# Kernel tuning notes

Measured on AMD Instinct MI355X. Metric: run time of the kernel, lower is better.

Reference implementation:

```python
import jax, jax.numpy as jnp
import numpy as np

B, DIM, L, H, W = 4, 128, 256, 8, 8
N = L * H * W
D_INNER, D_STATE, D_CONV, DT_RANK = 128, 8, 4, 8


def _ln(x, w, b, eps=1e-5):
    m = x.mean(-1, keepdims=True)
    v = ((x - m) ** 2).mean(-1, keepdims=True)
    return (x - m) * jax.lax.rsqrt(v + eps) * w + b


def _mamba_fusion(x, z_in, p, i):
    # x, z_in: (B, N, DIM). x drives the SSM; z_in provides the cross-modal gate.
    u = x @ p['Wx'][i]                                    # (B, N, D_INNER)
    z = z_in @ p['Wz'][i]                                 # (B, N, D_INNER)
    # causal depthwise conv1d along tokens, kernel D_CONV (torch pad=k-1 then truncate)
    up = jnp.pad(u, ((0, 0), (D_CONV - 1, 0), (0, 0)))
    w = p['conv_w'][i]                                    # (D_INNER, D_CONV)
    uc = sum(up[:, k:k + u.shape[1], :] * w[:, k] for k in range(D_CONV)) + p['conv_b'][i]
    uc = jax.nn.silu(uc)
    x_dbl = uc @ p['Wxproj'][i]                           # (B, N, DT_RANK + 2*D_STATE)
    dt_r, Bm, Cm = jnp.split(x_dbl, [DT_RANK, DT_RANK + D_STATE], axis=-1)
    dt = jax.nn.softplus(dt_r @ p['Wdt'][i] + p['bdt'][i])  # (B, N, D_INNER)
    A = -jnp.exp(p['A_log'][i])                           # (D_INNER, D_STATE)
    dA = jnp.exp(dt[..., None] * A)                       # (B, N, D_INNER, D_STATE)
    dBu = dt[..., None] * Bm[:, :, None, :] * uc[..., None]

    def step(h, inp):
        dA_t, dBu_t, C_t = inp
        h = dA_t * h + dBu_t                              # (B, D_INNER, D_STATE)
        return h, jnp.einsum('bds,bs->bd', h, C_t)

    h0 = jnp.zeros((u.shape[0], D_INNER, D_STATE), u.dtype)
    _, ys = jax.lax.scan(step, h0, (dA.swapaxes(0, 1), dBu.swapaxes(0, 1), Cm.swapaxes(0, 1)))
    y = ys.swapaxes(0, 1) + p['Dp'][i] * uc
    y = y * jax.nn.silu(z)
    return y @ p['Wout_m'][i] + p['bout_m'][i]


def _cross_block(in0, in1, p, i):
    skip = in0
    a = _ln(in0, p['ln0_w'][i], p['ln0_b'][i])
    b = _ln(in1, p['ln1_w'][i], p['ln1_b'][i])
    return skip + _mamba_fusion(a, b, p, i)


def setup_inputs() -> dict:
    key = jax.random.key(0)
    ks = jax.random.split(key, 16)
    s_in = 1.0 / np.sqrt(DIM)
    s_di = 1.0 / np.sqrt(D_INNER)
    inp = {
        'front': jax.random.normal(ks[0], (B, DIM, L, H, W), jnp.float32),
        'back': jax.random.normal(ks[1], (B, DIM, L, H, W), jnp.float32),
        'ln0_w': jnp.ones((2, DIM), jnp.float32),
        'ln0_b': jnp.zeros((2, DIM), jnp.float32),
        'ln1_w': jnp.ones((2, DIM), jnp.float32),
        'ln1_b': jnp.zeros((2, DIM), jnp.float32),
        'Wx': jax.random.normal(ks[2], (2, DIM, D_INNER), jnp.float32) * s_in,
        'Wz': jax.random.normal(ks[3], (2, DIM, D_INNER), jnp.float32) * s_in,
        'conv_w': jax.random.normal(ks[4], (2, D_INNER, D_CONV), jnp.float32) * 0.5,
        'conv_b': jnp.zeros((2, D_INNER), jnp.float32),
        'Wxproj': jax.random.normal(ks[5], (2, D_INNER, DT_RANK + 2 * D_STATE), jnp.float32) * s_di,
        'Wdt': jax.random.normal(ks[6], (2, DT_RANK, D_INNER), jnp.float32) * (1.0 / np.sqrt(DT_RANK)),
        'bdt': jnp.full((2, D_INNER), -4.6, jnp.float32),  # softplus^-1(~0.01)
        'A_log': jnp.broadcast_to(jnp.log(jnp.arange(1, D_STATE + 1, dtype=jnp.float32)), (2, D_INNER, D_STATE)).copy(),
        'Dp': jnp.ones((2, D_INNER), jnp.float32),
        'Wout_m': jax.random.normal(ks[7], (2, D_INNER, DIM), jnp.float32) * s_di,
        'bout_m': jnp.zeros((2, DIM), jnp.float32),
        'Wout': jax.random.normal(ks[8], (DIM, DIM), jnp.float32) * s_in,
        'bout': jnp.zeros((DIM,), jnp.float32),
    }
    return inp


def reference(front, back, ln0_w, ln0_b, ln1_w, ln1_b, Wx, Wz, conv_w, conv_b,
              Wxproj, Wdt, bdt, A_log, Dp, Wout_m, bout_m, Wout, bout):
    p = dict(ln0_w=ln0_w, ln0_b=ln0_b, ln1_w=ln1_w, ln1_b=ln1_b, Wx=Wx, Wz=Wz,
             conv_w=conv_w, conv_b=conv_b, Wxproj=Wxproj, Wdt=Wdt, bdt=bdt,
             A_log=A_log, Dp=Dp, Wout_m=Wout_m, bout_m=bout_m)
    ff = front.reshape(B, DIM, N).swapaxes(1, 2)          # (B, N, DIM)
    bf = back.reshape(B, DIM, N).swapaxes(1, 2)
    f_fus = _cross_block(ff, bf, p, 0)
    b_fus = _cross_block(bf, ff, p, 1)
    fusion = ((f_fus + b_fus) * 0.5) @ Wout + bout
    return fusion.swapaxes(1, 2).reshape(B, DIM, L, H, W)
```

## Files before the change

kernel.cpp:

```cpp
#include <hip/hip_runtime.h>

#define DEV static __device__ __forceinline__

typedef short s16x8 __attribute__((ext_vector_type(8)));
typedef float f32x4 __attribute__((ext_vector_type(4)));
typedef unsigned short u16;

DEV float b2f(u16 u){ return __uint_as_float(((unsigned int)u) << 16); }
DEV u16 f2b(float f){
  unsigned int x = __float_as_uint(f);
  x += 0x7fffu + ((x >> 16) & 1u);
  return (u16)(x >> 16);
}
DEV float silu_f(float x){ return x * __builtin_amdgcn_rcpf(1.f + __expf(-x)); }
DEV float softplus_f(float x){ return (x > 15.f) ? x : __logf(1.f + __expf(x)); }
DEV bool detf32(const void* lnw){ return *(const unsigned int*)lnw == 0x3F800000u; }
DEV float ldin(const void* p, long long i, bool f){
  return f ? ((const float*)p)[i] : b2f(((const u16*)p)[i]);
}

static constexpr int BATCH = 4;
static constexpr int NSEQ  = 16384;
static constexpr int RTOT  = BATCH * NSEQ;
static constexpr int GCH   = 256;
static constexpr int DIRSZ = BATCH*GCH*128*8;

DEV int swz(int row, int col){ return (row << 7) + (col ^ ((row & 7) << 3)); }

__global__ __launch_bounds__(256) void k_setup(
                        const void* ln0w, const void* ln0b, const void* ln1w, const void* ln1b,
                        const void* Wx, const void* Wz, const void* Wxp, const void* Wdt,
                        const void* bdt, const void* Alog, const void* convw, const void* convb,
                        const void* Dpr, const void* Woutm, const void* boutm,
                        const void* Wout, const void* bout,
                        u16* Wuz, u16* WdtBC, u16* Wcat, u16* WoutT,
                        float* buz, float* bdtf, float* bcat, float* boutf,
                        float* Aexp, float* convwF, float* convbF, float* DpF)
{
  bool f = detf32(ln0w);
  int tid = blockIdx.x * 256 + threadIdx.x;
  int gs  = gridDim.x * 256;
  for (int idx = tid; idx < 2*256*128; idx += gs){
    int d = idx >> 15; int n = (idx >> 7) & 255; int k = idx & 127;
    float wv;
    if (n < 128) wv = ldin(ln0w, d*128+k, f) * ldin(Wx, (long long)(d*128+k)*128 + n, f);
    else         wv = ldin(ln1w, (1-d)*128+k, f) * ldin(Wz, (long long)((1-d)*128+k)*128 + (n-128), f);
    Wuz[idx] = f2b(wv);
  }
  for (int idx = tid; idx < 2*256; idx += gs){
    int d = idx >> 8; int n = idx & 255;
    float s = 0.f;
    if (n < 128){
      for (int k = 0; k < 128; ++k)
        s += ldin(ln0b, d*128+k, f) * ldin(Wx, (long long)(d*128+k)*128 + n, f);
    } else {
      for (int k = 0; k < 128; ++k)
        s += ldin(ln1b, (1-d)*128+k, f) * ldin(Wz, (long long)((1-d)*128+k)*128 + (n-128), f);
    }
    buz[idx] = s;
  }
  for (int idx = tid; idx < 2*128; idx += gs)
    bdtf[idx] = ldin(bdt, idx, f);
  for (int idx = tid; idx < 2*144*128; idx += gs){
    int i = idx / (144*128); int rem = idx % (144*128); int n = rem >> 7; int k = rem & 127;
    if (n < 128){
      float s = 0.f;
      for (int j = 0; j < 8; ++j)
        s += ldin(Wxp, (long long)(i*128+k)*24 + j, f) * ldin(Wdt, (long long)(i*8+j)*128 + n, f);
      WdtBC[idx] = f2b(s);
    } else {
      WdtBC[idx] = f2b(ldin(Wxp, (long long)(i*128+k)*24 + (n - 120), f));
    }
  }
  for (int idx = tid; idx < 128*256; idx += gs){
    int n = idx >> 8; int k = idx & 255;
    Wcat[idx] = f2b(ldin(Woutm, (long long)k*128 + n, f));
  }
  for (int idx = tid; idx < 128*128; idx += gs){
    int n = idx >> 7, k = idx & 127;
    WoutT[idx] = f2b(ldin(Wout, (long long)k*128 + n, f));
  }
  for (int idx = tid; idx < 128; idx += gs){
    bcat[idx]  = ldin(boutm, idx, f) + ldin(boutm, 128 + idx, f);
    boutf[idx] = ldin(bout, idx, f);
  }
  for (int idx = tid; idx < 2*128*8; idx += gs)
    Aexp[idx] = -expf(ldin(Alog, idx, f));
  for (int idx = tid; idx < 2*128*4; idx += gs)
    convwF[idx] = ldin(convw, idx, f);
  for (int idx = tid; idx < 2*128; idx += gs){
    convbF[idx] = ldin(convb, idx, f);
    DpF[idx]   = ldin(Dpr, idx, f);
  }
}

__global__ __launch_bounds__(256) void k_ln(const void* front, const void* back, const void* ln0w,
                                            u16* xf, u16* xb, u16* sfbh)
{
  bool fF = detf32(ln0w);
  __shared__ u16 Af[64][130];
  __shared__ u16 Ab[64][130];
  __shared__ float Mf[64], Rf[64], Mb[64], Rb[64];
  int tid = threadIdx.x;
  long long r0 = (long long)blockIdx.x * 64;
  int b  = (int)(r0 >> 14);
  int n0 = (int)(r0 & 16383);
  if (fF){
    const float* fp = (const float*)front;
    const float* bp = (const float*)back;
    for (int it = 0; it < 8; ++it){
      int d = it*16 + (tid >> 4);
      int t = (tid & 15) * 4;
      long long gi = ((long long)(b*128 + d))*NSEQ + n0 + t;
      float4 vf = *(const float4*)&fp[gi];
      float4 vb = *(const float4*)&bp[gi];
      Af[t+0][d] = f2b(vf.x); Af[t+1][d] = f2b(vf.y);
      Af[t+2][d] = f2b(vf.z); Af[t+3][d] = f2b(vf.w);
      Ab[t+0][d] = f2b(vb.x); Ab[t+1][d] = f2b(vb.y);
      Ab[t+2][d] = f2b(vb.z); Ab[t+3][d] = f2b(vb.w);
    }
  } else {
    const u16* fp = (const u16*)front;
    const u16* bp = (const u16*)back;
    for (int it = 0; it < 4; ++it){
      int d = it*32 + (tid >> 3);
      int t = (tid & 7) * 8;
      long long gi = ((long long)(b*128 + d))*NSEQ + n0 + t;
      uint4 vf = *(const uint4*)&fp[gi];
      uint4 vb = *(const uint4*)&bp[gi];
      Af[t+0][d] = (u16)vf.x; Af[t+1][d] = (u16)(vf.x>>16);
      Af[t+2][d] = (u16)vf.y; Af[t+3][d] = (u16)(vf.y>>16);
      Af[t+4][d] = (u16)vf.z; Af[t+5][d] = (u16)(vf.z>>16);
      Af[t+6][d] = (u16)vf.w; Af[t+7][d] = (u16)(vf.w>>16);
      Ab[t+0][d] = (u16)vb.x; Ab[t+1][d] = (u16)(vb.x>>16);
      Ab[t+2][d] = (u16)vb.y; Ab[t+3][d] = (u16)(vb.y>>16);
      Ab[t+4][d] = (u16)vb.z; Ab[t+5][d] = (u16)(vb.z>>16);
      Ab[t+6][d] = (u16)vb.w; Ab[t+7][d] = (u16)(vb.w>>16);
    }
  }
  __syncthreads();
  {
    int t = tid >> 2, sub = tid & 3;
    float s = 0.f, ss = 0.f, s2 = 0.f, ss2 = 0.f;
    for (int k = 0; k < 32; ++k){
      float v = b2f(Af[t][sub*32 + k]); s  += v; ss  += v*v;
      float w = b2f(Ab[t][sub*32 + k]); s2 += w; ss2 += w*w;
    }
    for (int m = 1; m < 4; m <<= 1){
      s  += __shfl_xor(s,  m, 64); ss  += __shfl_xor(ss,  m, 64);
      s2 += __shfl_xor(s2, m, 64); ss2 += __shfl_xor(ss2, m, 64);
    }
    if (sub == 0){
      float mf = s  * (1.f/128.f); float vf = ss  * (1.f/128.f) - mf*mf;
      Mf[t] = mf; Rf[t] = rsqrtf(vf + 1e-5f);
      float mb = s2 * (1.f/128.f); float vb = ss2 * (1.f/128.f) - mb*mb;
      Mb[t] = mb; Rb[t] = rsqrtf(vb + 1e-5f);
    }
  }
  __syncthreads();
  for (int it = 0; it < 8; ++it){
    int t = it*8 + (tid >> 5);
    int c = (tid & 31) * 4;
    float mf = Mf[t], rf = Rf[t], mb = Mb[t], rb = Rb[t];
    float f0 = b2f(Af[t][c+0]), f1 = b2f(Af[t][c+1]), f2 = b2f(Af[t][c+2]), f3 = b2f(Af[t][c+3]);
    float g0 = b2f(Ab[t][c+0]), g1 = b2f(Ab[t][c+1]), g2 = b2f(Ab[t][c+2]), g3 = b2f(Ab[t][c+3]);
    ushort4 xo, zo, so;
    xo.x = f2b((f0-mf)*rf); xo.y = f2b((f1-mf)*rf); xo.z = f2b((f2-mf)*rf); xo.w = f2b((f3-mf)*rf);
    zo.x = f2b((g0-mb)*rb); zo.y = f2b((g1-mb)*rb); zo.z = f2b((g2-mb)*rb); zo.w = f2b((g3-mb)*rb);
    so.x = f2b(f0+g0); so.y = f2b(f1+g1); so.z = f2b(f2+g2); so.w = f2b(f3+g3);
    long long o = (r0 + t)*128 + c;
    *(ushort4*)&xf[o] = xo;
    *(ushort4*)&xb[o] = zo;
    *(ushort4*)&sfbh[o] = so;
  }
}

__global__ __launch_bounds__(256) void k_guz(const u16* __restrict__ xf,
                                             const u16* __restrict__ xb,
                                             const u16* __restrict__ Wuz,
                                             const float* __restrict__ buz,
                                             u16* __restrict__ u0, u16* __restrict__ u1,
                                             u16* __restrict__ z0, u16* __restrict__ z1)
{
  int dir = blockIdx.y;
  const u16* A = dir ? xb : xf;
  const u16* Wt = Wuz + dir*256*128;
  const float* bias = buz + dir*256;
  u16* outU = dir ? u1 : u0;
  u16* outZ = dir ? z0 : z1;
  __shared__ u16 Wl[256][72];
  __shared__ u16 Al[64][72];
  int tid = threadIdx.x;
  long long r0 = (long long)blockIdx.x * 64;
  int w = tid >> 6, lane = tid & 63;
  int q = lane >> 4, m = lane & 15;
  f32x4 acc[16];
  #pragma unroll
  for (int ct = 0; ct < 16; ++ct) acc[ct] = (f32x4){0.f,0.f,0.f,0.f};
  for (int kp = 0; kp < 2; ++kp){
    if (kp) __syncthreads();
    for (int ci = tid; ci < 256*8; ci += 256){
      int n = ci >> 3, c8 = ci & 7;
      *(uint4*)&Wl[n][c8*8] = *(const uint4*)&Wt[n*128 + kp*64 + c8*8];
    }
    for (int ci = tid; ci < 64*8; ci += 256){
      int rl = ci >> 3, c8 = ci & 7;
      *(uint4*)&Al[rl][c8*8] = *(const uint4*)&A[(r0 + rl)*128 + kp*64 + c8*8];
    }
    __syncthreads();
    #pragma unroll
    for (int kt = 0; kt < 2; ++kt){
      s16x8 af = *(const s16x8*)&Al[w*16 + m][kt*32 + q*8];
      #pragma unroll
      for (int ct = 0; ct < 16; ++ct){
        s16x8 bf = *(const s16x8*)&Wl[ct*16 + m][kt*32 + q*8];
        acc[ct] = __builtin_amdgcn_mfma_f32_16x16x32_bf16(af, bf, acc[ct], 0, 0, 0);
      }
    }
  }
  #pragma unroll
  for (int ct = 0; ct < 16; ++ct){
    int col = ct*16 + m;
    #pragma unroll
    for (int i = 0; i < 4; ++i){
      long long r = r0 + w*16 + q*4 + i;
      float v = acc[ct][i] + bias[col];
      if (col < 128) outU[r*128 + col] = f2b(v);
      else           outZ[r*128 + (col - 128)] = f2b(silu_f(v));
    }
  }
}

__global__ __launch_bounds__(256, 3) void k_cps(const u16* __restrict__ u0p,
                                             const u16* __restrict__ u1p,
                                             const float* __restrict__ convwF,
                                             const float* __restrict__ convbF,
                                             const u16* __restrict__ WdtBC,
                                             const float* __restrict__ bdtf,
                                             const float* __restrict__ Aexp,
                                             u16* __restrict__ uc0p, u16* __restrict__ uc1p,
                                             u16* __restrict__ yg,
                                             float* __restrict__ BCg,
                                             float* __restrict__ P, float* __restrict__ Q)
{
  __shared__ __align__(16) u16 AlF[64*128];
  __shared__ __align__(16) u16 WlF[144*128];
  int dir = blockIdx.y;
  const u16* u = dir ? u1p : u0p;
  u16* ucb = dir ? uc1p : uc0p;
  const u16* Wt = WdtBC + dir*18432;
  const float* bias = bdtf + dir*128;
  u16* dtb = yg + dir*128;
  float* BC = BCg + (long long)dir*RTOT*16;
  int tid = threadIdx.x;
  long long r0 = (long long)blockIdx.x * 64;
  int b  = (int)(r0 >> 14);
  int n0 = (int)(r0 & 16383);
  for (int ci = tid; ci < 144*16; ci += 256){
    int n = ci >> 4, c8 = ci & 15;
    *(uint4*)&WlF[(n << 7) + ((c8 ^ (n & 7)) << 3)] = *(const uint4*)&Wt[n*128 + c8*8];
  }
  {
    int c = tid & 127, h = tid >> 7;
    const float* wp = &convwF[(dir*128 + c)*4];
    float w0 = wp[0], w1 = wp[1], w2 = wp[2], w3 = wp[3];
    float cb = convbF[dir*128 + c];
    int t0 = h*32;
    const u16* up = u + (long long)b*NSEQ*128 + c;
    int nbase = n0 + t0;
    float win0 = (nbase-3 >= 0) ? b2f(up[(long long)(nbase-3)*128]) : 0.f;
    float win1 = (nbase-2 >= 0) ? b2f(up[(long long)(nbase-2)*128]) : 0.f;
    float win2 = (nbase-1 >= 0) ? b2f(up[(long long)(nbase-1)*128]) : 0.f;
    #pragma unroll
    for (int t = 0; t < 32; ++t){
      float cur = b2f(up[(long long)(nbase + t)*128]);
      float a = win0*w0 + win1*w1 + win2*w2 + cur*w3 + cb;
      u16 s = f2b(silu_f(a));
      AlF[swz(t0 + t, c)] = s;
      ucb[(r0 + t0 + t)*128 + c] = s;
      win0 = win1; win1 = win2; win2 = cur;
    }
  }
  __syncthreads();
  int w = tid >> 6, lane = tid & 63;
  int q = lane >> 4, m = lane & 15;
  f32x4 acc[9];
  #pragma unroll
  for (int ct = 0; ct < 9; ++ct) acc[ct] = (f32x4){0.f,0.f,0.f,0.f};
  #pragma unroll
  for (int kt = 0; kt < 4; ++kt){
    int sc = (kt*32 + q*8) ^ ((m & 7) << 3);
    s16x8 af = *(const s16x8*)&AlF[((w*16 + m) << 7) + sc];
    #pragma unroll
    for (int ct = 0; ct < 9; ++ct){
      s16x8 bf = *(const s16x8*)&WlF[((ct*16 + m) << 7) + sc];
      acc[ct] = __builtin_amdgcn_mfma_f32_16x16x32_bf16(af, bf, acc[ct], 0, 0, 0);
    }
  }
  __syncthreads();
  u16* Dl = WlF;
  float* BCl = (float*)&WlF[64*128];
  #pragma unroll
  for (int ct = 0; ct < 9; ++ct){
    int col = ct*16 + m;
    #pragma unroll
    for (int i = 0; i < 4; ++i){
      int rl = w*16 + q*4 + i;
      long long r = r0 + rl;
      float v = acc[ct][i];
      if (col < 128){
        u16 dv = f2b(softplus_f(v + bias[col]));
        dtb[r*256 + col] = dv;
        Dl[swz(rl, col)] = dv;
      } else {
        BC[r*16 + (col - 128)] = v;
        BCl[rl*16 + (col - 128)] = v;
      }
    }
  }
  __syncthreads();
  {
    int c = tid & 127, sh = tid >> 7;
    int g = (int)(r0 & 16383) >> 6;
    int base = sh*4;
    float Ac[4], Pr[4], H[4];
    bool fast = true;
    #pragma unroll
    for (int j = 0; j < 4; ++j){
      Ac[j] = Aexp[(dir*128 + c)*8 + base + j];
      fast = fast && (fabsf(Ac[j] + (float)(base + j + 1)) < 2e-4f);
      Pr[j] = 1.f; H[j] = 0.f;
    }
    if (fast){
      for (int t = 0; t < 64; ++t){
        int ce = swz(t, c);
        float d  = b2f(Dl[ce]);
        float uu = b2f(AlF[ce]);
        float du = d * uu;
        float E  = __expf(-d);
        float E2 = E*E, E3 = E2*E, E4 = E2*E2;
        float M  = base ? E4 : 1.f;
        float dA0 = M*E, dA1 = M*E2, dA2 = M*E3, dA3 = M*E4;
        H[0] = dA0*H[0] + du*BCl[t*16 + base+0]; Pr[0] *= dA0;
        H[1] = dA1*H[1] + du*BCl[t*16 + base+1]; Pr[1] *= dA1;
        H[2] = dA2*H[2] + du*BCl[t*16 + base+2]; Pr[2] *= dA2;
        H[3] = dA3*H[3] + du*BCl[t*16 + base+3]; Pr[3] *= dA3;
      }
    } else {
      for (int t = 0; t < 64; ++t){
        int ce = swz(t, c);
        float d  = b2f(Dl[ce]);
        float uu = b2f(AlF[ce]);
        float du = d * uu;
        #pragma unroll
        for (int j = 0; j < 4; ++j){
          float dA = __expf(d * Ac[j]);
          H[j]  = dA*H[j] + du*BCl[t*16 + base + j];
          Pr[j] *= dA;
        }
      }
    }
    long long o = (long long)dir*DIRSZ + (((long long)b*GCH + g)*128 + c)*8 + base;
    *(float4*)&P[o] = make_float4(Pr[0],Pr[1],Pr[2],Pr[3]);
    *(float4*)&Q[o] = make_float4(H[0],H[1],H[2],H[3]);
  }
}

__global__ __launch_bounds__(64) void k_scan2(const float* __restrict__ P,
                                              const float* __restrict__ Q,
                                              float* __restrict__ hinit)
{
  int idx = blockIdx.x*64 + threadIdx.x;
  int dir = idx >> 12;
  int rem = idx & 4095;
  int b  = rem >> 10;
  int cs = rem & 1023;
  long long base = (long long)dir*DIRSZ + (long long)b*GCH*1024 + cs;
  float h = 0.f;
  for (int g = 0; g < GCH; g += 8){
    long long o = base + (long long)g*1024;
    float p[8], qv[8];
    #pragma unroll
    for (int j = 0; j < 8; ++j){ p[j] = P[o + j*1024]; qv[j] = Q[o + j*1024]; }
    #pragma unroll
    for (int j = 0; j < 8; ++j){
      hinit[o + j*1024] = h;
      h = p[j]*h + qv[j];
    }
  }
}

__global__ __launch_bounds__(256) void k_scan3(const u16* __restrict__ uc0p,
                                               const u16* __restrict__ uc1p,
                                               const float* __restrict__ BCg,
                                               const float* __restrict__ hinit,
                                               const u16* __restrict__ z0p,
                                               const u16* __restrict__ z1p,
                                               const float* __restrict__ DpF,
                                               const float* __restrict__ Aexp,
                                               u16* yg)
{
  __shared__ float Bl[128][8];
  __shared__ float Cl[128][8];
  int dir = blockIdx.y;
  const u16* uc = dir ? uc1p : uc0p;
  const u16* zs = dir ? z1p : z0p;
  const float* BC = BCg + (long long)dir*RTOT*16;
  int tid = threadIdx.x;
  int gp = blockIdx.x & 127;
  int b  = blockIdx.x >> 7;
  long long tokbase = (long long)b*NSEQ + gp*128;
  for (int idx = tid; idx < 128*8; idx += 256){
    int row = idx >> 3, s = idx & 7;
    Bl[row][s] = BC[(tokbase + row)*16 + s];
    Cl[row][s] = BC[(tokbase + row)*16 + 8 + s];
  }
  __syncthreads();
  int c = tid & 127;
  int gh = tid >> 7;
  int g = gp*2 + gh;
  int doff = dir*128;
  float Ac[8], H[8];
  long long ho = (long long)dir*DIRSZ + (((long long)b*GCH + g)*128 + c)*8;
  float4 h0 = *(const float4*)&hinit[ho];
  float4 h1 = *(const float4*)&hinit[ho + 4];
  H[0]=h0.x; H[1]=h0.y; H[2]=h0.z; H[3]=h0.w;
  H[4]=h1.x; H[5]=h1.y; H[6]=h1.z; H[7]=h1.w;
  bool fast = true;
  #pragma unroll
  for (int s = 0; s < 8; ++s){
    Ac[s] = Aexp[(dir*128 + c)*8 + s];
    fast = fast && (fabsf(Ac[s] + (float)(s + 1)) < 2e-4f);
  }
  float dpc = DpF[dir*128 + c];
  long long rbase = (long long)b*NSEQ + g*64;
  if (fast){
    for (int t = 0; t < 64; ++t){
      long long r = rbase + t;
      float d  = b2f(yg[r*256 + doff + c]);
      float uu = b2f(uc[r*128 + c]);
      float du = d * uu;
      int rowl = gh*64 + t;
      float E  = __expf(-d);
      float E2 = E*E, E3 = E2*E, E4 = E2*E2;
      float dA[8] = {E, E2, E3, E4, E4*E, E4*E2, E4*E3, E4*E4};
      float y = 0.f;
      #pragma unroll
      for (int s = 0; s < 8; ++s){
        H[s] = dA[s]*H[s] + du*Bl[rowl][s];
        y += H[s]*Cl[rowl][s];
      }
      float zv = b2f(zs[r*128 + c]);
      yg[r*256 + doff + c] = f2b((y + dpc*uu) * zv);
    }
  } else {
    for (int t = 0; t < 64; ++t){
      long long r = rbase + t;
      float d  = b2f(yg[r*256 + doff + c]);
      float uu = b2f(uc[r*128 + c]);
      float du = d * uu;
      int rowl = gh*64 + t;
      float y = 0.f;
      #pragma unroll
      for (int s = 0; s < 8; ++s){
        float dA = __expf(d * Ac[s]);
        H[s] = dA*H[s] + du*Bl[rowl][s];
        y += H[s]*Cl[rowl][s];
      }
      float zv = b2f(zs[r*128 + c]);
      yg[r*256 + doff + c] = f2b((y + dpc*uu) * zv);
    }
  }
}

__global__ __launch_bounds__(256) void k_tail(const u16* __restrict__ yg,
                                              const u16* __restrict__ Wcat,
                                              const float* __restrict__ bcat,
                                              const u16* __restrict__ sfbh,
                                              const u16* __restrict__ WoutT,
                                              const float* __restrict__ boutf,
                                              void* outp, const void* dflag)
{
  __shared__ u16 Wl[128][136];
  __shared__ u16 Al[64][136];
  __shared__ u16 Sl[64][136];
  int tid = threadIdx.x;
  long long r0 = (long long)blockIdx.x * 64;
  int w = tid >> 6, lane = tid & 63;
  int q = lane >> 4, m = lane & 15;
  f32x4 acc[8];
  #pragma unroll
  for (int ct = 0; ct < 8; ++ct) acc[ct] = (f32x4){0.f,0.f,0.f,0.f};
  for (int kp = 0; kp < 2; ++kp){
    if (kp) __syncthreads();
    for (int ci = tid; ci < 128*16; ci += 256){
      int n = ci >> 4, c8 = ci & 15;
      *(uint4*)&Wl[n][c8*8] = *(const uint4*)&Wcat[n*256 + kp*128 + c8*8];
    }
    for (int ci = tid; ci < 64*16; ci += 256){
      int rl = ci >> 4, c8 = ci & 15;
      *(uint4*)&Al[rl][c8*8] = *(const uint4*)&yg[(r0 + rl)*256 + kp*128 + c8*8];
    }
    __syncthreads();
    #pragma unroll
    for (int kt = 0; kt < 4; ++kt){
      s16x8 af = *(const s16x8*)&Al[w*16 + m][kt*32 + q*8];
      #pragma unroll
      for (int ct = 0; ct < 8; ++ct){
        s16x8 bf = *(const s16x8*)&Wl[ct*16 + m][kt*32 + q*8];
        acc[ct] = __builtin_amdgcn_mfma_f32_16x16x32_bf16(af, bf, acc[ct], 0, 0, 0);
      }
    }
  }
  #pragma unroll
  for (int ct = 0; ct < 8; ++ct){
    int col = ct*16 + m;
    #pragma unroll
    for (int i = 0; i < 4; ++i){
      int rl = w*16 + q*4 + i;
      long long r = r0 + rl;
      Sl[rl][col] = f2b(acc[ct][i] + bcat[col] + b2f(sfbh[r*128 + col]));
    }
  }
  __syncthreads();
  for (int ci = tid; ci < 128*16; ci += 256){
    int n = ci >> 4, c8 = ci & 15;
    *(uint4*)&Wl[n][c8*8] = *(const uint4*)&WoutT[n*128 + c8*8];
  }
  __syncthreads();
  f32x4 acc2[8];
  #pragma unroll
  for (int ct = 0; ct < 8; ++ct) acc2[ct] = (f32x4){0.f,0.f,0.f,0.f};
  #pragma unroll
  for (int kt = 0; kt < 4; ++kt){
    s16x8 af = *(const s16x8*)&Sl[w*16 + m][kt*32 + q*8];
    #pragma unroll
    for (int ct = 0; ct < 8; ++ct){
      s16x8 bf = *(const s16x8*)&Wl[ct*16 + m][kt*32 + q*8];
      acc2[ct] = __builtin_amdgcn_mfma_f32_16x16x32_bf16(af, bf, acc2[ct], 0, 0, 0);
    }
  }
  u16* Tl = &Al[0][0];
  #pragma unroll
  for (int ct = 0; ct < 8; ++ct){
    int col = ct*16 + m;
    #pragma unroll
    for (int i = 0; i < 4; ++i){
      int rl = w*16 + q*4 + i;
      Tl[col*68 + rl] = f2b(0.5f*acc2[ct][i] + boutf[col]);
    }
  }
  __syncthreads();
  long long b = r0 >> 14; long long tok0 = r0 & 16383;
  bool fo = detf32(dflag);
  if (fo){
    float* of = (float*)outp;
    for (int idx = tid; idx < 128*16; idx += 256){
      int n = idx >> 4; int t0 = (idx & 15)*4;
      float4 v;
      v.x = b2f(Tl[n*68 + t0+0]); v.y = b2f(Tl[n*68 + t0+1]);
      v.z = b2f(Tl[n*68 + t0+2]); v.w = b2f(Tl[n*68 + t0+3]);
      *(float4*)&of[(((long long)(b*128 + n)) << 14) + tok0 + t0] = v;
    }
  } else {
    u16* ob = (u16*)outp;
    for (int idx = tid; idx < 128*16; idx += 256){
      int n = idx >> 4; int t0 = (idx & 15)*4;
      ushort4 v;
      v.x = Tl[n*68 + t0+0]; v.y = Tl[n*68 + t0+1];
      v.z = Tl[n*68 + t0+2]; v.w = Tl[n*68 + t0+3];
      *(ushort4*)&ob[(((long long)(b*128 + n)) << 14) + tok0 + t0] = v;
    }
  }
}

extern "C" void kernel_launch(void* const* d_in, const int* in_sizes, int n_in,
                              void* d_out, int out_size, void* d_ws, size_t ws_size,
                              hipStream_t stream)
{
  (void)in_sizes; (void)n_in; (void)out_size; (void)ws_size;
  const void* front = d_in[0];
  const void* back  = d_in[1];
  const void* ln0w  = d_in[2];
  const void* ln0b  = d_in[3];
  const void* ln1w  = d_in[4];
  const void* ln1b  = d_in[5];
  const void* Wx    = d_in[6];
  const void* Wz    = d_in[7];
  const void* convw = d_in[8];
  const void* convb = d_in[9];
  const void* Wxp   = d_in[10];
  const void* Wdt   = d_in[11];
  const void* bdt   = d_in[12];
  const void* Alog  = d_in[13];
  const void* Dpr   = d_in[14];
  const void* Woutm = d_in[15];
  const void* boutm = d_in[16];
  const void* Wout  = d_in[17];
  const void* bout  = d_in[18];

  char* p = (char*)d_ws;
  auto alloc = [&](size_t bytes) -> void* {
    void* q = (void*)p; p += (bytes + 255) & ~(size_t)255; return q;
  };
  u16*   xf    = (u16*)  alloc((size_t)RTOT*128*2);
  u16*   xb    = (u16*)  alloc((size_t)RTOT*128*2);
  u16*   sfbh  = (u16*)  alloc((size_t)RTOT*128*2);
  u16*   u0    = (u16*)  alloc((size_t)RTOT*128*2);
  u16*   u1    = (u16*)  alloc((size_t)RTOT*128*2);
  u16*   z0    = (u16*)  alloc((size_t)RTOT*128*2);
  u16*   z1    = (u16*)  alloc((size_t)RTOT*128*2);
  float* BC    = (float*)alloc((size_t)2*RTOT*16*4);
  float* Pb    = (float*)alloc((size_t)2*DIRSZ*4);
  float* Qb    = (float*)alloc((size_t)2*DIRSZ*4);
  float* hin   = (float*)alloc((size_t)2*DIRSZ*4);
  u16*   yg    = (u16*)  alloc((size_t)RTOT*256*2);
  u16*   Wuz   = (u16*)  alloc(2*256*128*2);
  u16*   WdtBC = (u16*)  alloc(2*144*128*2);
  u16*   Wcat  = (u16*)  alloc(128*256*2);
  u16*   WoutT = (u16*)  alloc(128*128*2);
  float* buz   = (float*)alloc(2*256*4);
  float* bdtf  = (float*)alloc(2*128*4);
  float* bcat  = (float*)alloc(128*4);
  float* boutf = (float*)alloc(128*4);
  float* Aexp  = (float*)alloc(2*128*8*4);
  float* convwF= (float*)alloc(2*128*4*4);
  float* convbF= (float*)alloc(2*128*4);
  float* DpF   = (float*)alloc(2*128*4);

  k_setup<<<128,256,0,stream>>>(ln0w,ln0b,ln1w,ln1b,Wx,Wz,Wxp,Wdt,bdt,Alog,convw,convb,Dpr,
                                Woutm,boutm,Wout,bout,
                                Wuz,WdtBC,Wcat,WoutT,buz,bdtf,bcat,boutf,Aexp,
                                convwF,convbF,DpF);
  k_ln<<<RTOT/64,256,0,stream>>>(front,back,ln0w,xf,xb,sfbh);

  dim3 g2(RTOT/64, 2);
  k_guz<<<g2,256,0,stream>>>(xf, xb, Wuz, buz, u0, u1, z0, z1);
  k_cps<<<g2,256,0,stream>>>(u0, u1, convwF, convbF, WdtBC, bdtf, Aexp,
                             xf, xb, yg, BC, Pb, Qb);
  k_scan2<<<128,64,0,stream>>>(Pb, Qb, hin);
  dim3 g3(BATCH*GCH/2, 2);
  k_scan3<<<g3,256,0,stream>>>(xf, xb, BC, hin, z0, z1, DpF, Aexp, yg);
  k_tail<<<RTOT/64,256,0,stream>>>(yg, Wcat, bcat, sfbh, WoutT, boutf, d_out, ln0w);
}
```

Before: 329.4 us.

## Fuse chunk-local scan output into conv kernel and apply carry correction in tail

```diff
diff --git a/kernel.cpp b/kernel.cpp
--- a/kernel.cpp
+++ b/kernel.cpp
@@ -1,4 +1,5 @@
 #include <hip/hip_runtime.h>
+#include <hip/hip_fp16.h>
 
 #define DEV static __device__ __forceinline__
 
@@ -12,6 +13,8 @@
   x += 0x7fffu + ((x >> 16) & 1u);
   return (u16)(x >> 16);
 }
+DEV u16 f2h(float f){ __half h = __float2half(f); u16 u; __builtin_memcpy(&u, &h, 2); return u; }
+DEV float h2f(u16 u){ __half h; __builtin_memcpy(&h, &u, 2); return __half2float(h); }
 DEV float silu_f(float x){ return x * __builtin_amdgcn_rcpf(1.f + __expf(-x)); }
 DEV float softplus_f(float x){ return (x > 15.f) ? x : __logf(1.f + __expf(x)); }
 DEV bool detf32(const void* lnw){ return *(const unsigned int*)lnw == 0x3F800000u; }
@@ -175,7 +178,7 @@
   }
 }
 
-__global__ __launch_bounds__(256) void k_guz(const u16* __restrict__ xf,
+__global__ __launch_bounds__(256, 4) void k_guz(const u16* __restrict__ xf,
                                              const u16* __restrict__ xb,
                                              const u16* __restrict__ Wuz,
                                              const float* __restrict__ buz,
@@ -188,8 +191,8 @@
   const float* bias = buz + dir*256;
   u16* outU = dir ? u1 : u0;
   u16* outZ = dir ? z0 : z1;
-  __shared__ u16 Wl[256][72];
-  __shared__ u16 Al[64][72];
+  __shared__ __align__(16) u16 Wl[256*64];
+  __shared__ __align__(16) u16 Al[64*64];
   int tid = threadIdx.x;
   long long r0 = (long long)blockIdx.x * 64;
   int w = tid >> 6, lane = tid & 63;
@@ -201,19 +204,20 @@
     if (kp) __syncthreads();
     for (int ci = tid; ci < 256*8; ci += 256){
       int n = ci >> 3, c8 = ci & 7;
-      *(uint4*)&Wl[n][c8*8] = *(const uint4*)&Wt[n*128 + kp*64 + c8*8];
+      *(uint4*)&Wl[(n << 6) + ((c8 ^ (n & 7)) << 3)] = *(const uint4*)&Wt[n*128 + kp*64 + c8*8];
     }
     for (int ci = tid; ci < 64*8; ci += 256){
       int rl = ci >> 3, c8 = ci & 7;
-      *(uint4*)&Al[rl][c8*8] = *(const uint4*)&A[(r0 + rl)*128 + kp*64 + c8*8];
+      *(uint4*)&Al[(rl << 6) + ((c8 ^ (rl & 7)) << 3)] = *(const uint4*)&A[(r0 + rl)*128 + kp*64 + c8*8];
     }
     __syncthreads();
     #pragma unroll
     for (int kt = 0; kt < 2; ++kt){
-      s16x8 af = *(const s16x8*)&Al[w*16 + m][kt*32 + q*8];
+      int sc = ((kt*4 + q) ^ (m & 7)) << 3;
+      s16x8 af = *(const s16x8*)&Al[((w*16 + m) << 6) + sc];
       #pragma unroll
       for (int ct = 0; ct < 16; ++ct){
-        s16x8 bf = *(const s16x8*)&Wl[ct*16 + m][kt*32 + q*8];
+        s16x8 bf = *(const s16x8*)&Wl[((ct*16 + m) << 6) + sc];
         acc[ct] = __builtin_amdgcn_mfma_f32_16x16x32_bf16(af, bf, acc[ct], 0, 0, 0);
       }
     }
@@ -238,8 +242,9 @@
                                              const u16* __restrict__ WdtBC,
                                              const float* __restrict__ bdtf,
                                              const float* __restrict__ Aexp,
-                                             u16* __restrict__ uc0p, u16* __restrict__ uc1p,
-                                             u16* __restrict__ yg,
+                                             const float* __restrict__ DpF,
+                                             u16* __restrict__ yl0, u16* __restrict__ yl1,
+                                             u16* __restrict__ Eg,
                                              float* __restrict__ BCg,
                                              float* __restrict__ P, float* __restrict__ Q)
 {
@@ -247,10 +252,8 @@
   __shared__ __align__(16) u16 WlF[144*128];
   int dir = blockIdx.y;
   const u16* u = dir ? u1p : u0p;
-  u16* ucb = dir ? uc1p : uc0p;
   const u16* Wt = WdtBC + dir*18432;
   const float* bias = bdtf + dir*128;
-  u16* dtb = yg + dir*128;
   float* BC = BCg + (long long)dir*RTOT*16;
   int tid = threadIdx.x;
   long long r0 = (long long)blockIdx.x * 64;
@@ -275,9 +278,7 @@
     for (int t = 0; t < 32; ++t){
       float cur = b2f(up[(long long)(nbase + t)*128]);
       float a = win0*w0 + win1*w1 + win2*w2 + cur*w3 + cb;
-      u16 s = f2b(silu_f(a));
-      AlF[swz(t0 + t, c)] = s;
-      ucb[(r0 + t0 + t)*128 + c] = s;
+      AlF[swz(t0 + t, c)] = f2b(silu_f(a));
       win0 = win1; win1 = win2; win2 = cur;
     }
   }
@@ -309,42 +310,52 @@
       long long r = r0 + rl;
       float v = acc[ct][i];
       if (col < 128){
-        u16 dv = f2b(softplus_f(v + bias[col]));
-        dtb[r*256 + col] = dv;
-        Dl[swz(rl, col)] = dv;
+        Dl[swz(rl, col)] = f2b(softplus_f(v + bias[col]));
       } else {
-        BC[r*16 + (col - 128)] = v;
         BCl[rl*16 + (col - 128)] = v;
-      }
-    }
-  }
-  __syncthreads();
-  {
-    int c = tid & 127, sh = tid >> 7;
+        if (col >= 136) BC[r*16 + (col - 128)] = v;
+      }
+    }
+  }
+  __syncthreads();
+  if (tid < 128){
+    int c = tid;
     int g = (int)(r0 & 16383) >> 6;
-    int base = sh*4;
-    float Ac[4], Pr[4], H[4];
+    float Ac[8], H[8];
     bool fast = true;
     #pragma unroll
-    for (int j = 0; j < 4; ++j){
-      Ac[j] = Aexp[(dir*128 + c)*8 + base + j];
-      fast = fast && (fabsf(Ac[j] + (float)(base + j + 1)) < 2e-4f);
-      Pr[j] = 1.f; H[j] = 0.f;
-    }
+    for (int s = 0; s < 8; ++s){
+      Ac[s] = Aexp[(dir*128 + c)*8 + s];
+      fast = fast && (fabsf(Ac[s] + (float)(s + 1)) < 2e-4f);
+      H[s] = 0.f;
+    }
+    float dpc = DpF[dir*128 + c];
+    u16* ylArr = dir ? yl1 : yl0;
+    u16* EArr  = Eg + (size_t)dir*((size_t)RTOT*128);
+    long long sb = r0*128 + c;
+    float PE = 1.f, sd = 0.f;
     if (fast){
       for (int t = 0; t < 64; ++t){
         int ce = swz(t, c);
         float d  = b2f(Dl[ce]);
         float uu = b2f(AlF[ce]);
         float du = d * uu;
-        float E  = __expf(-d);
-        float E2 = E*E, E3 = E2*E, E4 = E2*E2;
-        float M  = base ? E4 : 1.f;
-        float dA0 = M*E, dA1 = M*E2, dA2 = M*E3, dA3 = M*E4;
-        H[0] = dA0*H[0] + du*BCl[t*16 + base+0]; Pr[0] *= dA0;
-        H[1] = dA1*H[1] + du*BCl[t*16 + base+1]; Pr[1] *= dA1;
-        H[2] = dA2*H[2] + du*BCl[t*16 + base+2]; Pr[2] *= dA2;
-        H[3] = dA3*H[3] + du*BCl[t*16 + base+3]; Pr[3] *= dA3;
+        float E1 = __expf(-d);
+        PE *= E1;
+        float E2=E1*E1, E3=E2*E1, E4=E2*E2;
+        float E5=E4*E1, E6=E4*E2, E7=E4*E3, E8=E4*E4;
+        float4 b0 = *(const float4*)&BCl[t*16];
+        float4 b1 = *(const float4*)&BCl[t*16 + 4];
+        float4 c0 = *(const float4*)&BCl[t*16 + 8];
+        float4 c1 = *(const float4*)&BCl[t*16 + 12];
+        H[0]=E1*H[0]+du*b0.x; H[1]=E2*H[1]+du*b0.y;
+        H[2]=E3*H[2]+du*b0.z; H[3]=E4*H[3]+du*b0.w;
+        H[4]=E5*H[4]+du*b1.x; H[5]=E6*H[5]+du*b1.y;
+        H[6]=E7*H[6]+du*b1.z; H[7]=E8*H[7]+du*b1.w;
+        float y = H[0]*c0.x + H[1]*c0.y + H[2]*c0.z + H[3]*c0.w
+                + H[4]*c1.x + H[5]*c1.y + H[6]*c1.z + H[7]*c1.w;
+        ylArr[sb + (long long)t*128] = f2b(y + dpc*uu);
+        EArr [sb + (long long)t*128] = f2h(PE);
       }
     } else {
       for (int t = 0; t < 64; ++t){
@@ -352,17 +363,32 @@
         float d  = b2f(Dl[ce]);
         float uu = b2f(AlF[ce]);
         float du = d * uu;
+        sd += d;
+        float y = 0.f;
         #pragma unroll
-        for (int j = 0; j < 4; ++j){
-          float dA = __expf(d * Ac[j]);
-          H[j]  = dA*H[j] + du*BCl[t*16 + base + j];
-          Pr[j] *= dA;
+        for (int s = 0; s < 8; ++s){
+          float dA = __expf(d * Ac[s]);
+          H[s] = dA*H[s] + du*BCl[t*16 + s];
+          y += H[s]*BCl[t*16 + 8 + s];
         }
-      }
-    }
-    long long o = (long long)dir*DIRSZ + (((long long)b*GCH + g)*128 + c)*8 + base;
-    *(float4*)&P[o] = make_float4(Pr[0],Pr[1],Pr[2],Pr[3]);
-    *(float4*)&Q[o] = make_float4(H[0],H[1],H[2],H[3]);
+        ylArr[sb + (long long)t*128] = f2b(y + dpc*uu);
+        EArr [sb + (long long)t*128] = f2b(sd);
+      }
+    }
+    long long o = (long long)dir*DIRSZ + (((long long)b*GCH + g)*128 + c)*8;
+    float Pr[8];
+    if (fast){
+      float P2=PE*PE, P3=P2*PE, P4=P2*P2;
+      Pr[0]=PE; Pr[1]=P2; Pr[2]=P3; Pr[3]=P4;
+      Pr[4]=P4*PE; Pr[5]=P4*P2; Pr[6]=P4*P3; Pr[7]=P4*P4;
+    } else {
+      #pragma unroll
+      for (int s = 0; s < 8; ++s) Pr[s] = __expf(sd * Ac[s]);
+    }
+    *(float4*)&P[o]     = make_float4(Pr[0],Pr[1],Pr[2],Pr[3]);
+    *(float4*)&P[o + 4] = make_float4(Pr[4],Pr[5],Pr[6],Pr[7]);
+    *(float4*)&Q[o]     = make_float4(H[0],H[1],H[2],H[3]);
+    *(float4*)&Q[o + 4] = make_float4(H[4],H[5],H[6],H[7]);
   }
 }
 
@@ -390,90 +416,14 @@
   }
 }
 
-__global__ __launch_bounds__(256) void k_scan3(const u16* __restrict__ uc0p,
-                                               const u16* __restrict__ uc1p,
-                                               const float* __restrict__ BCg,
-                                               const float* __restrict__ hinit,
-                                               const u16* __restrict__ z0p,
-                                               const u16* __restrict__ z1p,
-                                               const float* __restrict__ DpF,
-                                               const float* __restrict__ Aexp,
-                                               u16* yg)
-{
-  __shared__ float Bl[128][8];
-  __shared__ float Cl[128][8];
-  int dir = blockIdx.y;
-  const u16* uc = dir ? uc1p : uc0p;
-  const u16* zs = dir ? z1p : z0p;
-  const float* BC = BCg + (long long)dir*RTOT*16;
-  int tid = threadIdx.x;
-  int gp = blockIdx.x & 127;
-  int b  = blockIdx.x >> 7;
-  long long tokbase = (long long)b*NSEQ + gp*128;
-  for (int idx = tid; idx < 128*8; idx += 256){
-    int row = idx >> 3, s = idx & 7;
-    Bl[row][s] = BC[(tokbase + row)*16 + s];
-    Cl[row][s] = BC[(tokbase + row)*16 + 8 + s];
-  }
-  __syncthreads();
-  int c = tid & 127;
-  int gh = tid >> 7;
-  int g = gp*2 + gh;
-  int doff = dir*128;
-  float Ac[8], H[8];
-  long long ho = (long long)dir*DIRSZ + (((long long)b*GCH + g)*128 + c)*8;
-  float4 h0 = *(const float4*)&hinit[ho];
-  float4 h1 = *(const float4*)&hinit[ho + 4];
-  H[0]=h0.x; H[1]=h0.y; H[2]=h0.z; H[3]=h0.w;
-  H[4]=h1.x; H[5]=h1.y; H[6]=h1.z; H[7]=h1.w;
-  bool fast = true;
-  #pragma unroll
-  for (int s = 0; s < 8; ++s){
-    Ac[s] = Aexp[(dir*128 + c)*8 + s];
-    fast = fast && (fabsf(Ac[s] + (float)(s + 1)) < 2e-4f);
-  }
-  float dpc = DpF[dir*128 + c];
-  long long rbase = (long long)b*NSEQ + g*64;
-  if (fast){
-    for (int t = 0; t < 64; ++t){
-      long long r = rbase + t;
-      float d  = b2f(yg[r*256 + doff + c]);
-      float uu = b2f(uc[r*128 + c]);
-      float du = d * uu;
-      int rowl = gh*64 + t;
-      float E  = __expf(-d);
-      float E2 = E*E, E3 = E2*E, E4 = E2*E2;
-      float dA[8] = {E, E2, E3, E4, E4*E, E4*E2, E4*E3, E4*E4};
-      float y = 0.f;
-      #pragma unroll
-      for (int s = 0; s < 8; ++s){
-        H[s] = dA[s]*H[s] + du*Bl[rowl][s];
-        y += H[s]*Cl[rowl][s];
-      }
-      float zv = b2f(zs[r*128 + c]);
-      yg[r*256 + doff + c] = f2b((y + dpc*uu) * zv);
-    }
-  } else {
-    for (int t = 0; t < 64; ++t){
-      long long r = rbase + t;
-      float d  = b2f(yg[r*256 + doff + c]);
-      float uu = b2f(uc[r*128 + c]);
-      float du = d * uu;
-      int rowl = gh*64 + t;
-      float y = 0.f;
-      #pragma unroll
-      for (int s = 0; s < 8; ++s){
-        float dA = __expf(d * Ac[s]);
-        H[s] = dA*H[s] + du*Bl[rowl][s];
-        y += H[s]*Cl[rowl][s];
-      }
-      float zv = b2f(zs[r*128 + c]);
-      yg[r*256 + doff + c] = f2b((y + dpc*uu) * zv);
-    }
-  }
-}
-
-__global__ __launch_bounds__(256) void k_tail(const u16* __restrict__ yg,
+__global__ __launch_bounds__(256, 3) void k_tail(const u16* __restrict__ yl0,
+                                              const u16* __restrict__ yl1,
+                                              const u16* __restrict__ Eg,
+                                              const float* __restrict__ BCg,
+                                              const float* __restrict__ hinit,
+                                              const u16* __restrict__ z0p,
+                                              const u16* __restrict__ z1p,
+                                              const float* __restrict__ Aexp,
                                               const u16* __restrict__ Wcat,
                                               const float* __restrict__ bcat,
                                               const u16* __restrict__ sfbh,
@@ -483,11 +433,13 @@
 {
   __shared__ u16 Wl[128][136];
   __shared__ u16 Al[64][136];
-  __shared__ u16 Sl[64][136];
   int tid = threadIdx.x;
   long long r0 = (long long)blockIdx.x * 64;
+  int bb = (int)(r0 >> 14);
+  int g  = ((int)(r0 & 16383)) >> 6;
   int w = tid >> 6, lane = tid & 63;
   int q = lane >> 4, m = lane & 15;
+  int pc = tid & 127, rh = tid >> 7;
   f32x4 acc[8];
   #pragma unroll
   for (int ct = 0; ct < 8; ++ct) acc[ct] = (f32x4){0.f,0.f,0.f,0.f};
@@ -497,9 +449,60 @@
       int n = ci >> 4, c8 = ci & 15;
       *(uint4*)&Wl[n][c8*8] = *(const uint4*)&Wcat[n*256 + kp*128 + c8*8];
     }
-    for (int ci = tid; ci < 64*16; ci += 256){
-      int rl = ci >> 4, c8 = ci & 15;
-      *(uint4*)&Al[rl][c8*8] = *(const uint4*)&yg[(r0 + rl)*256 + kp*128 + c8*8];
+    {
+      const u16* ylv = kp ? yl1 : yl0;
+      const u16* Ev  = Eg + (size_t)kp*((size_t)RTOT*128);
+      const u16* zs  = kp ? z1p : z0p;
+      const float* BCd = BCg + (size_t)kp*((size_t)RTOT*16);
+      float h[8];
+      {
+        long long ho = (long long)kp*DIRSZ + (((long long)bb*GCH + g)*128 + pc)*8;
+        float4 h0v = *(const float4*)&hinit[ho];
+        float4 h1v = *(const float4*)&hinit[ho + 4];
+        h[0]=h0v.x; h[1]=h0v.y; h[2]=h0v.z; h[3]=h0v.w;
+        h[4]=h1v.x; h[5]=h1v.y; h[6]=h1v.z; h[7]=h1v.w;
+      }
+      float Ac[8]; bool fastc = true;
+      #pragma unroll
+      for (int s = 0; s < 8; ++s){
+        Ac[s] = Aexp[(kp*128 + pc)*8 + s];
+        fastc = fastc && (fabsf(Ac[s] + (float)(s + 1)) < 2e-4f);
+      }
+      long long sb = (r0 + rh*32)*128 + pc;
+      if (fastc){
+        for (int i = 0; i < 32; ++i){
+          int t = rh*32 + i;
+          long long r = r0 + t;
+          float4 c0 = *(const float4*)&BCd[r*16 + 8];
+          float4 c1 = *(const float4*)&BCd[r*16 + 12];
+          float yl = b2f(ylv[sb + (long long)i*128]);
+          float E  = h2f(Ev [sb + (long long)i*128]);
+          float corr =          h[7]*c1.w;
+          corr = corr*E + h[6]*c1.z;
+          corr = corr*E + h[5]*c1.y;
+          corr = corr*E + h[4]*c1.x;
+          corr = corr*E + h[3]*c0.w;
+          corr = corr*E + h[2]*c0.z;
+          corr = corr*E + h[1]*c0.y;
+          corr = corr*E + h[0]*c0.x;
+          corr *= E;
+          float zz = b2f(zs[sb + (long long)i*128]);
+          Al[t][pc] = f2b((yl + corr)*zz);
+        }
+      } else {
+        for (int i = 0; i < 32; ++i){
+          int t = rh*32 + i;
+          long long r = r0 + t;
+          float yl = b2f(ylv[sb + (long long)i*128]);
+          float cd = b2f(Ev [sb + (long long)i*128]);
+          float corr = 0.f;
+          #pragma unroll
+          for (int s = 0; s < 8; ++s)
+            corr += h[s]*BCd[r*16 + 8 + s]*__expf(cd*Ac[s]);
+          float zz = b2f(zs[sb + (long long)i*128]);
+          Al[t][pc] = f2b((yl + corr)*zz);
+        }
+      }
     }
     __syncthreads();
     #pragma unroll
@@ -512,6 +515,7 @@
       }
     }
   }
+  __syncthreads();
   #pragma unroll
   for (int ct = 0; ct < 8; ++ct){
     int col = ct*16 + m;
@@ -519,10 +523,9 @@
     for (int i = 0; i < 4; ++i){
       int rl = w*16 + q*4 + i;
       long long r = r0 + rl;
-      Sl[rl][col] = f2b(acc[ct][i] + bcat[col] + b2f(sfbh[r*128 + col]));
-    }
-  }
-  __syncthreads();
+      Al[rl][col] = f2b(acc[ct][i] + bcat[col] + b2f(sfbh[r*128 + col]));
+    }
+  }
   for (int ci = tid; ci < 128*16; ci += 256){
     int n = ci >> 4, c8 = ci & 15;
     *(uint4*)&Wl[n][c8*8] = *(const uint4*)&WoutT[n*128 + c8*8];
@@ -533,14 +536,15 @@
   for (int ct = 0; ct < 8; ++ct) acc2[ct] = (f32x4){0.f,0.f,0.f,0.f};
   #pragma unroll
   for (int kt = 0; kt < 4; ++kt){
-    s16x8 af = *(const s16x8*)&Sl[w*16 + m][kt*32 + q*8];
+    s16x8 af = *(const s16x8*)&Al[w*16 + m][kt*32 + q*8];
     #pragma unroll
     for (int ct = 0; ct < 8; ++ct){
       s16x8 bf = *(const s16x8*)&Wl[ct*16 + m][kt*32 + q*8];
       acc2[ct] = __builtin_amdgcn_mfma_f32_16x16x32_bf16(af, bf, acc2[ct], 0, 0, 0);
     }
   }
-  u16* Tl = &Al[0][0];
+  __syncthreads();
+  u16* Tl = &Wl[0][0];
   #pragma unroll
   for (int ct = 0; ct < 8; ++ct){
     int col = ct*16 + m;
@@ -614,7 +618,7 @@
   float* Pb    = (float*)alloc((size_t)2*DIRSZ*4);
   float* Qb    = (float*)alloc((size_t)2*DIRSZ*4);
   float* hin   = (float*)alloc((size_t)2*DIRSZ*4);
-  u16*   yg    = (u16*)  alloc((size_t)RTOT*256*2);
+  u16*   Eg    = (u16*)  alloc((size_t)RTOT*256*2);
   u16*   Wuz   = (u16*)  alloc(2*256*128*2);
   u16*   WdtBC = (u16*)  alloc(2*144*128*2);
   u16*   Wcat  = (u16*)  alloc(128*256*2);
@@ -636,10 +640,9 @@
 
   dim3 g2(RTOT/64, 2);
   k_guz<<<g2,256,0,stream>>>(xf, xb, Wuz, buz, u0, u1, z0, z1);
-  k_cps<<<g2,256,0,stream>>>(u0, u1, convwF, convbF, WdtBC, bdtf, Aexp,
-                             xf, xb, yg, BC, Pb, Qb);
+  k_cps<<<g2,256,0,stream>>>(u0, u1, convwF, convbF, WdtBC, bdtf, Aexp, DpF,
+                             xf, xb, Eg, BC, Pb, Qb);
   k_scan2<<<128,64,0,stream>>>(Pb, Qb, hin);
-  dim3 g3(BATCH*GCH/2, 2);
-  k_scan3<<<g3,256,0,stream>>>(xf, xb, BC, hin, z0, z1, DpF, Aexp, yg);
-  k_tail<<<RTOT/64,256,0,stream>>>(yg, Wcat, bcat, sfbh, WoutT, boutf, d_out, ln0w);
-}
+  k_tail<<<RTOT/64,256,0,stream>>>(xf, xb, Eg, BC, hin, z0, z1, Aexp,
+                                   Wcat, bcat, sfbh, WoutT, boutf, d_out, ln0w);
+}
```

New measurement: 342.8 us. 4.1% more time.
